# Kernel tuning notes

Hardware: AMD Instinct MI355X
Metric: run time of the kernel (lower is better)

The kernel has to match this reference:

```python
import jax, jax.numpy as jnp
import numpy as np

EPS = 1e-8


def setup_inputs() -> dict:
    key = jax.random.key(0)
    ks = jax.random.split(key, 11)
    N, D_OBS, D_AC, K = 2_000_000, 32, 16, 128
    H = int(1.66 * K)  # 212, matches int(1.66*k) in the torch module
    s = 0.05
    return {
        "obs": jax.random.normal(ks[0], (N, D_OBS), dtype=jnp.float32),
        "acs": jax.random.normal(ks[1], (N, D_AC), dtype=jnp.float32),
        "x": jax.random.normal(ks[2], (D_OBS,), dtype=jnp.float32),
        "w_in": jax.random.normal(ks[3], (H, K), dtype=jnp.float32) * s,
        "b_in": jax.random.normal(ks[4], (H,), dtype=jnp.float32) * s,
        "w2": jax.random.normal(ks[5], (H, H), dtype=jnp.float32) * s,
        "b2": jax.random.normal(ks[6], (H,), dtype=jnp.float32) * s,
        "w3": jax.random.normal(ks[7], (H, H), dtype=jnp.float32) * s,
        "b3": jax.random.normal(ks[8], (H,), dtype=jnp.float32) * s,
        "w_out": jax.random.normal(ks[9], (K, H), dtype=jnp.float32) * s,
        "b_out": jax.random.normal(ks[10], (K,), dtype=jnp.float32) * s,
        "k": K,
    }


def reference(obs, acs, x, w_in, b_in, w2, b2, w3, b3, w_out, b_out, k):
    # cosine distance between every obs row and the query x: [N]
    xn = x * jax.lax.rsqrt(jnp.sum(x * x) + EPS)
    obs_nrm = jax.lax.rsqrt(jnp.sum(obs * obs, axis=1) + EPS)  # [N]
    cos_sim = (obs @ xn) * obs_nrm                              # [N]
    cos_dist = 1.0 - cos_sim                                    # [N]

    # top-k smallest distances (argpartition equivalent, sorted ascending)
    neg_vals, idx = jax.lax.top_k(-cos_dist, k)                 # [k], [k]
    k_cos_dist = -neg_vals                                      # [k]
    k_actions = acs[idx]                                        # [k, D_ac]

    # tiny MLP on the k distances -> softmax weights over the k neighbors
    h = jax.nn.relu(k_cos_dist @ w_in.T + b_in)
    h = jax.nn.relu(h @ w2.T + b2)
    h = jax.nn.relu(h @ w3.T + b3)
    weights = jax.nn.softmax(h @ w_out.T + b_out)               # [k]

    # weighted sum of the k neighbor actions -> [1, D_ac]
    out = jnp.sum(weights[:, None] * k_actions, axis=0, keepdims=True)
    return out
```

## Files before the change

### kernel.cpp

```cpp
#include <hip/hip_runtime.h>
#include <math.h>

#define NBIN 4096
#define CAPC 4096
#define KSEL 128
#define HDIM 212
#define DAC  16
#define EPSF 1e-8f
#define GRID1 2048

__global__ void k_init(const float* __restrict__ x, float* __restrict__ xn,
                       unsigned* __restrict__ hist, unsigned* __restrict__ meta) {
    int t = threadIdx.x;
    __shared__ float rs;
    if (t < 32) {
        float v = x[t];
        float s = v * v;
        #pragma unroll
        for (int o = 16; o >= 1; o >>= 1) s += __shfl_down(s, o);
        if (t == 0) rs = rsqrtf(s + EPSF);
    }
    __syncthreads();
    if (t < 32) xn[t] = x[t] * rs;
    for (int b = t; b < NBIN; b += blockDim.x) hist[b] = 0u;
    if (t < 8) meta[t] = 0u;
}

__global__ __launch_bounds__(256) void k_cos_hist(
        const float4* __restrict__ obs4, const float* __restrict__ xn,
        float* __restrict__ cosb, unsigned* __restrict__ hist, int N) {
    __shared__ unsigned lhist[NBIN];
    __shared__ float xs[32];
    for (int b = threadIdx.x; b < NBIN; b += 256) lhist[b] = 0u;
    if (threadIdx.x < 32) xs[threadIdx.x] = xn[threadIdx.x];
    __syncthreads();

    float4 X[8];
    #pragma unroll
    for (int q = 0; q < 8; q++)
        X[q] = make_float4(xs[4*q+0], xs[4*q+1], xs[4*q+2], xs[4*q+3]);

    const int stride = gridDim.x * blockDim.x;
    for (int row = blockIdx.x * blockDim.x + threadIdx.x; row < N; row += stride) {
        const float4* rp = obs4 + (size_t)row * 8;
        float4 v0 = rp[0], v1 = rp[1], v2 = rp[2], v3 = rp[3];
        float4 v4 = rp[4], v5 = rp[5], v6 = rp[6], v7 = rp[7];

        #define D4(v, q) ((v).x*X[q].x + (v).y*X[q].y + (v).z*X[q].z + (v).w*X[q].w)
        #define N4(v)    ((v).x*(v).x + (v).y*(v).y + (v).z*(v).z + (v).w*(v).w)
        float dA = D4(v0,0) + D4(v1,1);
        float dB = D4(v2,2) + D4(v3,3);
        float dC = D4(v4,4) + D4(v5,5);
        float dD = D4(v6,6) + D4(v7,7);
        float nA = N4(v0) + N4(v1);
        float nB = N4(v2) + N4(v3);
        float nC = N4(v4) + N4(v5);
        float nD = N4(v6) + N4(v7);
        #undef D4
        #undef N4
        float dot = (dA + dB) + (dC + dD);
        float nrm = (nA + nB) + (nC + nD);

        float cd = 1.0f - dot * rsqrtf(nrm + EPSF);
        cosb[row] = cd;
        unsigned u = __float_as_uint(cd);
        unsigned key = (u & 0x80000000u) ? ~u : (u | 0x80000000u);
        atomicAdd(&lhist[key >> 20], 1u);
    }

    __syncthreads();
    for (int b = threadIdx.x; b < NBIN; b += 256) {
        unsigned c = lhist[b];
        if (c) atomicAdd(&hist[b], c);
    }
}

__global__ __launch_bounds__(1024) void k_scan(const unsigned* __restrict__ hist,
                                               unsigned* __restrict__ meta, int K) {
    __shared__ unsigned psum[1024];
    int t = threadIdx.x;
    unsigned c[4];
    unsigned local = 0;
    #pragma unroll
    for (int q = 0; q < 4; q++) { c[q] = hist[4*t + q]; local += c[q]; }
    psum[t] = local;
    __syncthreads();
    for (int o = 1; o < 1024; o <<= 1) {
        unsigned v = (t >= o) ? psum[t - o] : 0u;
        __syncthreads();
        psum[t] += v;
        __syncthreads();
    }
    unsigned incl = psum[t];
    unsigned excl = incl - local;
    if (excl < (unsigned)K && (unsigned)K <= incl) {
        unsigned cum = excl;
        int B = 4*t;
        #pragma unroll
        for (int q = 0; q < 4; q++) {
            cum += c[q];
            if (cum >= (unsigned)K) { B = 4*t + q; break; }
        }
        meta[1] = (B >= NBIN - 1) ? 0xFFFFFFFFu : ((unsigned)(B + 1) << 20);
    }
}

__global__ __launch_bounds__(256) void k_compact(
        const float4* __restrict__ cos4, unsigned* __restrict__ meta,
        float* __restrict__ cval, int* __restrict__ cidx, int n4, int N) {
    unsigned keyHi = meta[1];
    int g = blockIdx.x * blockDim.x + threadIdx.x;
    if (g >= n4) return;
    float4 v = cos4[g];
    float vv[4] = {v.x, v.y, v.z, v.w};
    #pragma unroll
    for (int q = 0; q < 4; q++) {
        int i = g*4 + q;
        if (i < N) {
            unsigned u = __float_as_uint(vv[q]);
            unsigned key = (u & 0x80000000u) ? ~u : (u | 0x80000000u);
            if (key < keyHi) {
                unsigned pos = atomicAdd(&meta[0], 1u);
                if (pos < CAPC) { cval[pos] = vv[q]; cidx[pos] = i; }
            }
        }
    }
}

__global__ __launch_bounds__(512) void k_final(
        const float* __restrict__ cval, const int* __restrict__ cidx,
        const unsigned* __restrict__ meta, const float* __restrict__ acs,
        const float* __restrict__ w_in, const float* __restrict__ b_in,
        const float* __restrict__ w2, const float* __restrict__ b2,
        const float* __restrict__ w3, const float* __restrict__ b3,
        const float* __restrict__ w_out, const float* __restrict__ b_out,
        float* __restrict__ out) {
    __shared__ unsigned kv[CAPC];
    __shared__ int      idv[CAPC];
    __shared__ unsigned char act[CAPC];
    __shared__ unsigned hist2[256];
    __shared__ unsigned remArr[9];
    __shared__ unsigned pivB[8];
    __shared__ unsigned selB_sh;
    __shared__ unsigned scnt;
    __shared__ unsigned skey[KSEL];
    __shared__ int      sidx[KSEL];
    __shared__ float    sval[KSEL];
    __shared__ float d[KSEL];
    __shared__ int   id2[KSEL];
    __shared__ float h1[HDIM], h2[HDIM], h3[HDIM], lg[KSEL];
    __shared__ float smax_sh, rsum_sh;

    const int t = threadIdx.x;
    int M = (int)meta[0];
    if (M > CAPC) M = CAPC;

    for (int i = t; i < M; i += 512) {
        float v = cval[i];
        unsigned u = __float_as_uint(v);
        kv[i]  = (u & 0x80000000u) ? ~u : (u | 0x80000000u);
        idv[i] = cidx[i];
        act[i] = 1;
    }
    if (t == 0) remArr[0] = KSEL - 1;
    if (t < KSEL) {
        skey[t] = 0xFFFFFFFFu; sidx[t] = 0x7FFFFFFF; sval[t] = 0.f;
        d[t] = 0.f; id2[t] = 0;
    }
    __syncthreads();

    for (int r = 0; r < 8; r++) {
        if (t < 256) hist2[t] = 0u;
        __syncthreads();
        for (int i = t; i < M; i += 512) {
            if (act[i]) {
                unsigned b = (r < 4) ? ((kv[i] >> ((3-r)*8)) & 0xFFu)
                                     : (((unsigned)idv[i] >> ((7-r)*8)) & 0xFFu);
                atomicAdd(&hist2[b], 1u);
            }
        }
        __syncthreads();
        if (t < 64) {
            unsigned s0 = hist2[4*t], s1 = hist2[4*t+1],
                     s2 = hist2[4*t+2], s3 = hist2[4*t+3];
            unsigned tot = s0 + s1 + s2 + s3;
            unsigned sc = tot;
            #pragma unroll
            for (int o = 1; o < 64; o <<= 1) {
                unsigned v2 = __shfl_up(sc, o);
                if (t >= o) sc += v2;
            }
            unsigned cb = sc - tot;
            unsigned rm = remArr[r];
            unsigned ss[4] = {s0, s1, s2, s3};
            #pragma unroll
            for (int q = 0; q < 4; q++) {
                if (cb <= rm && rm < cb + ss[q]) {
                    selB_sh = 4*t + q;
                    pivB[r] = 4*t + q;
                    remArr[r+1] = rm - cb;
                }
                cb += ss[q];
            }
        }
        __syncthreads();
        unsigned sb = selB_sh;
        for (int i = t; i < M; i += 512) {
            if (act[i]) {
                unsigned b = (r < 4) ? ((kv[i] >> ((3-r)*8)) & 0xFFu)
                                     : (((unsigned)idv[i] >> ((7-r)*8)) & 0xFFu);
                if (b != sb) act[i] = 0;
            }
        }
        __syncthreads();
    }

    unsigned kvP = (pivB[0]<<24) | (pivB[1]<<16) | (pivB[2]<<8) | pivB[3];
    unsigned idP = (pivB[4]<<24) | (pivB[5]<<16) | (pivB[6]<<8) | pivB[7];
    if (t == 0) scnt = 0u;
    __syncthreads();

    for (int i = t; i < M; i += 512) {
        unsigned k = kv[i];
        unsigned ui = (unsigned)idv[i];
        if (k < kvP || (k == kvP && ui <= idP)) {
            unsigned p = atomicAdd(&scnt, 1u);
            if (p < KSEL) {
                skey[p] = k;
                sidx[p] = idv[i];
                unsigned u = (k & 0x80000000u) ? (k & 0x7FFFFFFFu) : ~k;
                sval[p] = __uint_as_float(u);
            }
        }
    }
    __syncthreads();

    if (t < KSEL) {
        unsigned mk = skey[t], mi = (unsigned)sidx[t];
        int rank = 0;
        for (int j = 0; j < KSEL; j++) {
            unsigned jk = skey[j], ji = (unsigned)sidx[j];
            rank += (jk < mk || (jk == mk && ji < mi)) ? 1 : 0;
        }
        d[rank] = sval[t];
        id2[rank] = sidx[t];
    }
    __syncthreads();

    if (t < HDIM) {
        float s = b_in[t];
        const float* wr = &w_in[t * KSEL];
        for (int j = 0; j < KSEL; j++) s += wr[j] * d[j];
        h1[t] = s > 0.f ? s : 0.f;
    }
    __syncthreads();
    if (t < HDIM) {
        float s = b2[t];
        const float* wr = &w2[t * HDIM];
        for (int j = 0; j < HDIM; j++) s += wr[j] * h1[j];
        h2[t] = s > 0.f ? s : 0.f;
    }
    __syncthreads();
    if (t < HDIM) {
        float s = b3[t];
        const float* wr = &w3[t * HDIM];
        for (int j = 0; j < HDIM; j++) s += wr[j] * h2[j];
        h3[t] = s > 0.f ? s : 0.f;
    }
    __syncthreads();
    if (t < KSEL) {
        float s = b_out[t];
        const float* wr = &w_out[t * HDIM];
        for (int j = 0; j < HDIM; j++) s += wr[j] * h3[j];
        lg[t] = s;
    }
    __syncthreads();

    if (t < 64) {
        float a = fmaxf(lg[t], lg[t + 64]);
        #pragma unroll
        for (int o = 32; o >= 1; o >>= 1) a = fmaxf(a, __shfl_xor(a, o));
        if (t == 0) smax_sh = a;
    }
    __syncthreads();
    if (t < KSEL) lg[t] = __expf(lg[t] - smax_sh);
    __syncthreads();
    if (t < 64) {
        float s = lg[t] + lg[t + 64];
        #pragma unroll
        for (int o = 32; o >= 1; o >>= 1) s += __shfl_xor(s, o);
        if (t == 0) rsum_sh = 1.0f / s;
    }
    __syncthreads();

    if (t < DAC) {
        float s = 0.f;
        for (int j = 0; j < KSEL; j++)
            s += lg[j] * acs[(size_t)id2[j] * DAC + t];
        out[t] = s * rsum_sh;
    }
}

extern "C" void kernel_launch(void* const* d_in, const int* in_sizes, int n_in,
                              void* d_out, int out_size, void* d_ws, size_t ws_size,
                              hipStream_t stream) {
    const float* obs   = (const float*)d_in[0];
    const float* acs   = (const float*)d_in[1];
    const float* x     = (const float*)d_in[2];
    const float* w_in  = (const float*)d_in[3];
    const float* b_in  = (const float*)d_in[4];
    const float* w2    = (const float*)d_in[5];
    const float* b2    = (const float*)d_in[6];
    const float* w3    = (const float*)d_in[7];
    const float* b3    = (const float*)d_in[8];
    const float* w_out = (const float*)d_in[9];
    const float* b_out = (const float*)d_in[10];
    float* out = (float*)d_out;

    int N = in_sizes[0] / 32;

    char* ws = (char*)d_ws;
    float*    xn   = (float*)ws;
    float*    cosb = (float*)(ws + 256);
    size_t histOff = 256 + (((size_t)N * 4 + 255) / 256) * 256;
    unsigned* hist = (unsigned*)(ws + histOff);
    unsigned* meta = (unsigned*)(ws + histOff + NBIN * 4);
    float*    cval = (float*)(ws + histOff + NBIN * 4 + 256);
    int*      cidx = (int*)(ws + histOff + NBIN * 4 + 256 + CAPC * 4);

    k_init<<<1, 256, 0, stream>>>(x, xn, hist, meta);

    k_cos_hist<<<GRID1, 256, 0, stream>>>((const float4*)obs, xn, cosb, hist, N);

    k_scan<<<1, 1024, 0, stream>>>(hist, meta, KSEL);

    int n4 = (N + 3) / 4;
    k_compact<<<(n4 + 255) / 256, 256, 0, stream>>>((const float4*)cosb, meta,
                                                    cval, cidx, n4, N);

    k_final<<<1, 512, 0, stream>>>(cval, cidx, meta, acs, w_in, b_in,
                                   w2, b2, w3, b3, w_out, b_out, out);
}
```

Baseline: 132.9 us.

## Fuse histogram threshold scan into compact kernel and scalarize query vector

Removes the single-block scan kernel launch and instead has every compact block redundantly compute the threshold bin from the global histogram with a 64-lane wave scan. The query vector is also forced into scalar registers via readfirstlane in the cosine kernel. This saves one launch and its serialization gap, but each of the roughly 2000 compact blocks now reads the 16 KB histogram, adding L2 traffic and per-block latency before compaction.

After: 164.7 us. 1.24x slower.

```diff
diff --git a/kernel.cpp b/kernel.cpp
--- a/kernel.cpp
+++ b/kernel.cpp
@@ -35,10 +35,10 @@
     if (threadIdx.x < 32) xs[threadIdx.x] = xn[threadIdx.x];
     __syncthreads();
 
-    float4 X[8];
+    float sx[32];
     #pragma unroll
-    for (int q = 0; q < 8; q++)
-        X[q] = make_float4(xs[4*q+0], xs[4*q+1], xs[4*q+2], xs[4*q+3]);
+    for (int q = 0; q < 32; q++)
+        sx[q] = __uint_as_float(__builtin_amdgcn_readfirstlane(__float_as_uint(xs[q])));
 
     const int stride = gridDim.x * blockDim.x;
     for (int row = blockIdx.x * blockDim.x + threadIdx.x; row < N; row += stride) {
@@ -46,7 +46,7 @@
         float4 v0 = rp[0], v1 = rp[1], v2 = rp[2], v3 = rp[3];
         float4 v4 = rp[4], v5 = rp[5], v6 = rp[6], v7 = rp[7];
 
-        #define D4(v, q) ((v).x*X[q].x + (v).y*X[q].y + (v).z*X[q].z + (v).w*X[q].w)
+        #define D4(v, q) ((v).x*sx[4*(q)+0] + (v).y*sx[4*(q)+1] + (v).z*sx[4*(q)+2] + (v).w*sx[4*(q)+3])
         #define N4(v)    ((v).x*(v).x + (v).y*(v).y + (v).z*(v).z + (v).w*(v).w)
         float dA = D4(v0,0) + D4(v1,1);
         float dB = D4(v2,2) + D4(v3,3);
@@ -75,41 +75,36 @@
     }
 }
 
-__global__ __launch_bounds__(1024) void k_scan(const unsigned* __restrict__ hist,
-                                               unsigned* __restrict__ meta, int K) {
-    __shared__ unsigned psum[1024];
+__global__ __launch_bounds__(256) void k_compact(
+        const float4* __restrict__ cos4, const unsigned* __restrict__ hist,
+        unsigned* __restrict__ meta,
+        float* __restrict__ cval, int* __restrict__ cidx, int n4, int N) {
+    __shared__ unsigned keyHi_sh;
     int t = threadIdx.x;
-    unsigned c[4];
-    unsigned local = 0;
-    #pragma unroll
-    for (int q = 0; q < 4; q++) { c[q] = hist[4*t + q]; local += c[q]; }
-    psum[t] = local;
-    __syncthreads();
-    for (int o = 1; o < 1024; o <<= 1) {
-        unsigned v = (t >= o) ? psum[t - o] : 0u;
-        __syncthreads();
-        psum[t] += v;
-        __syncthreads();
-    }
-    unsigned incl = psum[t];
-    unsigned excl = incl - local;
-    if (excl < (unsigned)K && (unsigned)K <= incl) {
-        unsigned cum = excl;
-        int B = 4*t;
+    if (t < 64) {
+        unsigned local = 0;
+        for (int q = 0; q < 64; q++) local += hist[64*t + q];
+        unsigned sc = local;
         #pragma unroll
-        for (int q = 0; q < 4; q++) {
-            cum += c[q];
-            if (cum >= (unsigned)K) { B = 4*t + q; break; }
-        }
-        meta[1] = (B >= NBIN - 1) ? 0xFFFFFFFFu : ((unsigned)(B + 1) << 20);
-    }
-}
-
-__global__ __launch_bounds__(256) void k_compact(
-        const float4* __restrict__ cos4, unsigned* __restrict__ meta,
-        float* __restrict__ cval, int* __restrict__ cidx, int n4, int N) {
-    unsigned keyHi = meta[1];
-    int g = blockIdx.x * blockDim.x + threadIdx.x;
+        for (int o = 1; o < 64; o <<= 1) {
+            unsigned v = __shfl_up(sc, o);
+            if (t >= o) sc += v;
+        }
+        unsigned excl = sc - local;
+        if (excl < KSEL && KSEL <= sc) {
+            unsigned cum = excl;
+            int B = 64*t;
+            for (int q = 0; q < 64; q++) {
+                cum += hist[64*t + q];
+                if (cum >= KSEL) { B = 64*t + q; break; }
+            }
+            keyHi_sh = (B >= NBIN - 1) ? 0xFFFFFFFFu : ((unsigned)(B + 1) << 20);
+        }
+    }
+    __syncthreads();
+    unsigned keyHi = keyHi_sh;
+
+    int g = blockIdx.x * blockDim.x + t;
     if (g >= n4) return;
     float4 v = cos4[g];
     float vv[4] = {v.x, v.y, v.z, v.w};
@@ -332,11 +327,9 @@
 
     k_cos_hist<<<GRID1, 256, 0, stream>>>((const float4*)obs, xn, cosb, hist, N);
 
-    k_scan<<<1, 1024, 0, stream>>>(hist, meta, KSEL);
-
     int n4 = (N + 3) / 4;
-    k_compact<<<(n4 + 255) / 256, 256, 0, stream>>>((const float4*)cosb, meta,
-                                                    cval, cidx, n4, N);
+    k_compact<<<(n4 + 255) / 256, 256, 0, stream>>>((const float4*)cosb, hist,
+                                                    meta, cval, cidx, n4, N);
 
     k_final<<<1, 512, 0, stream>>>(cval, cidx, meta, acs, w_in, b_in,
                                    w2, b2, w3, b3, w_out, b_out, out);
```
